# Optimization experiments

Hardware: AMD Instinct MI355X
Metric: run time of the kernel (lower is better)

## Reference

```python
import jax, jax.numpy as jnp
import numpy as np

N = 50000          # nodes (num_sensors)
E = 600000         # edges
IN_DIM = 75        # 3 * 25
DIMS = [(75, 128), (128, 128), (128, 32)]  # (in, out) per layer: in->hidden->hidden->bottleneck


def setup_inputs() -> dict:
    key = jax.random.key(0)
    ks = jax.random.split(key, 4 + 5 * len(DIMS))
    inp = {
        "x": jax.random.normal(ks[0], (N, IN_DIM), dtype=jnp.float32),
        "edge_index": jax.random.randint(ks[1], (2, E), 0, N, dtype=jnp.int64),
        "weight": jax.random.uniform(ks[2], (E,), dtype=jnp.float32),
        "sim": jax.random.normal(ks[3], (E, 2), dtype=jnp.float32),
    }
    i = 4
    for l, (cin, cout) in enumerate(DIMS):
        s = jnp.float32(1.0 / np.sqrt(cin))
        inp[f"wr{l}"] = jax.random.normal(ks[i + 0], (cin, cout), dtype=jnp.float32) * s  # real part of complex conv filter
        inp[f"wi{l}"] = jax.random.normal(ks[i + 1], (cin, cout), dtype=jnp.float32) * s  # imag part
        inp[f"cb{l}"] = jnp.zeros((cout,), dtype=jnp.float32)                              # conv bias
        inp[f"lw{l}"] = jax.random.normal(ks[i + 2], (cout, cin), dtype=jnp.float32) * s  # Linear weight (torch layout [out,in])
        inp[f"lb{l}"] = jnp.zeros((cout,), dtype=jnp.float32)                              # Linear bias
        i += 5
    return inp


def _layer(x, src, dst, cr, ci, wr, wi, cb, lw, lb):
    # ModeConvFast: gather source features, scale by complex edge coefficient
    # c = weight * (sim_r + i*sim_i), scatter-add to destination nodes,
    # project with complex filter W = wr + i*wi, keep real part, add bias.
    xs = x[src]                                   # [E, Cin] gather
    agg_r = jax.ops.segment_sum(xs * cr[:, None], dst, num_segments=N)  # [N, Cin]
    agg_i = jax.ops.segment_sum(xs * ci[:, None], dst, num_segments=N)  # [N, Cin]
    conv = agg_r @ wr - agg_i @ wi + cb           # real part of complex matmul
    return jax.nn.relu(conv + x @ lw.T + lb)      # conv(x,...) + lin(x), then relu


def reference(x, edge_index, weight, sim,
              wr0, wi0, cb0, lw0, lb0,
              wr1, wi1, cb1, lw1, lb1,
              wr2, wi2, cb2, lw2, lb2):
    src, dst = edge_index[0], edge_index[1]
    cr = weight * sim[:, 0]                       # [E] real edge coefficient
    ci = weight * sim[:, 1]                       # [E] imag edge coefficient
    layers = [
        (wr0, wi0, cb0, lw0, lb0),
        (wr1, wi1, cb1, lw1, lb1),
        (wr2, wi2, cb2, lw2, lb2),
    ]
    for p in layers:
        x = _layer(x, src, dst, cr, ci, *p)
    return x
```

## Files before the change

### kernel.cpp

```cpp
#include <hip/hip_runtime.h>

#define N_NODES 50000
#define N_EDGES 600000
#define E_PAD_MAX (N_EDGES + N_NODES * 7)

using bf16x8 = __attribute__((ext_vector_type(8))) short;
using f32x4  = __attribute__((ext_vector_type(4))) float;
typedef unsigned int uint32_tt;

__device__ __forceinline__ unsigned short f2bf(float f) {
    union { float f; unsigned int u; } v; v.f = f;
    unsigned int u = v.u;
    return (unsigned short)((u + 0x7fffu + ((u >> 16) & 1u)) >> 16);
}
__device__ __forceinline__ float bf2f(unsigned int h16) {
    union { unsigned int u; float f; } v; v.u = h16 << 16;
    return v.f;
}

__global__ void prep_kernel(
    const float* __restrict__ x0, unsigned short* __restrict__ xb,
    const float* __restrict__ wr0, const float* __restrict__ wi0,
    const float* __restrict__ lw0, unsigned short* __restrict__ BT0,
    const float* __restrict__ wr1, const float* __restrict__ wi1,
    const float* __restrict__ lw1, unsigned short* __restrict__ BT1,
    const float* __restrict__ wr2, const float* __restrict__ wi2,
    const float* __restrict__ lw2, unsigned short* __restrict__ BT2,
    int* __restrict__ cnt, uint2* __restrict__ edat, int n) {
    int tid = blockIdx.x * 256 + threadIdx.x;
    int nth = gridDim.x * 256;
    for (int i = tid; i < N_NODES; i += nth) cnt[i] = 0;
    uint2 z; z.x = 0u; z.y = 0u;
    for (int i = tid; i < E_PAD_MAX; i += nth) edat[i] = z;

    int i = tid;
    int nconv = n * 96;
    if (i < nconv) {
        int r = i / 96, c = i - r * 96;
        xb[i] = (c < 75) ? f2bf(x0[r * 75 + c]) : (unsigned short)0;
        return;
    }
    i -= nconv;
    if (i < 128 * 288) {
        int nn = i / 288, k = i - nn * 288;
        int part = k / 96, kk = k - part * 96;
        float v = 0.f;
        if (kk < 75) {
            if (part == 0)      v = wr0[kk * 128 + nn];
            else if (part == 1) v = -wi0[kk * 128 + nn];
            else                v = lw0[nn * 75 + kk];
        }
        BT0[i] = f2bf(v);
        return;
    }
    i -= 128 * 288;
    if (i < 128 * 384) {
        int nn = i / 384, k = i - nn * 384;
        int part = k >> 7, kk = k & 127;
        float v;
        if (part == 0)      v = wr1[kk * 128 + nn];
        else if (part == 1) v = -wi1[kk * 128 + nn];
        else                v = lw1[nn * 128 + kk];
        BT1[i] = f2bf(v);
        return;
    }
    i -= 128 * 384;
    if (i < 96 * 128) {
        int nn = i >> 7, k = i & 127;
        float v;
        if (nn < 32)      v = wr2[k * 32 + nn];
        else if (nn < 64) v = -wi2[k * 32 + (nn - 32)];
        else              v = lw2[(nn - 64) * 128 + k];
        BT2[i] = f2bf(v);
    }
}


__global__ void hist_kernel(const int* __restrict__ ei, int* __restrict__ cnt,
                            int* __restrict__ rank, int E) {
    int e = blockIdx.x * 256 + threadIdx.x;
    if (e < E) rank[e] = atomicAdd(&cnt[ei[E + e]], 1);
}

__global__ void scan1(const int* __restrict__ deg, int* __restrict__ out,
                      int* __restrict__ bsum, int n) {
    __shared__ int s[256];
    int t = threadIdx.x;
    int base = blockIdx.x * 1024 + t * 4;
    int v0 = (base + 0 < n) ? ((deg[base + 0] + 7) & ~7) : 0;
    int v1 = (base + 1 < n) ? ((deg[base + 1] + 7) & ~7) : 0;
    int v2 = (base + 2 < n) ? ((deg[base + 2] + 7) & ~7) : 0;
    int v3 = (base + 3 < n) ? ((deg[base + 3] + 7) & ~7) : 0;
    int tsum = v0 + v1 + v2 + v3;
    s[t] = tsum;
    __syncthreads();
    for (int off = 1; off < 256; off <<= 1) {
        int tmp = (t >= off) ? s[t - off] : 0;
        __syncthreads();
        s[t] += tmp;
        __syncthreads();
    }
    int excl = s[t] - tsum;
    if (base + 0 < n) out[base + 0] = excl;
    if (base + 1 < n) out[base + 1] = excl + v0;
    if (base + 2 < n) out[base + 2] = excl + v0 + v1;
    if (base + 3 < n) out[base + 3] = excl + v0 + v1 + v2;
    if (t == 255) bsum[blockIdx.x] = s[255];
}

__global__ void scan2(int* __restrict__ bsum, int nb) {
    if (threadIdx.x == 0 && blockIdx.x == 0) {
        int acc = 0;
        for (int i = 0; i < nb; ++i) { int v = bsum[i]; bsum[i] = acc; acc += v; }
        bsum[nb] = acc;
    }
}

__global__ void scan3(int* __restrict__ off, const int* __restrict__ bsum, int n, int nb) {
    int i = blockIdx.x * 256 + threadIdx.x;
    if (i < n) off[i] += bsum[i >> 10];
    if (i == n) off[n] = bsum[nb];
}

__global__ void scatter_kernel(const int* __restrict__ ei, const float* __restrict__ w,
                               const float* __restrict__ sim, const int* __restrict__ off,
                               const int* __restrict__ rank, uint2* __restrict__ edat,
                               int E) {
    int e = blockIdx.x * 256 + threadIdx.x;
    if (e >= E) return;
    int s = ei[e], d = ei[E + e];
    int p = off[d] + rank[e];
    float wt = w[e];
    uint2 m;
    m.x = (unsigned)s;
    m.y = (uint32_tt)f2bf(wt * sim[2 * e]) |
          ((uint32_tt)f2bf(wt * sim[2 * e + 1]) << 16);
    edat[p] = m;
}

template <int CU2>
__global__ __launch_bounds__(256) void agg_bf16(
    const uint32_tt* __restrict__ x, const int* __restrict__ off,
    const uint2* __restrict__ edat, uint32_tt* __restrict__ aggR,
    uint32_tt* __restrict__ aggI, int n) {
    int wave = threadIdx.x >> 6;
    int lane = threadIdx.x & 63;
    int node = __builtin_amdgcn_readfirstlane(blockIdx.x * 4 + wave);
    if (node >= n) return;
    int lc = (CU2 == 64) ? lane : (lane < CU2 ? lane : CU2 - 1);
    float arl = 0.f, arh = 0.f, ail = 0.f, aih = 0.f;
    int e0 = __builtin_amdgcn_readfirstlane(off[node]);
    int e1 = __builtin_amdgcn_readfirstlane(off[node + 1]);

    if (e0 < e1) {
        uint2 mn[8];
        int sc[8]; float crc[8], cic[8];
        uint32_tt wc[8];
        {
            uint2 m0[8];
#pragma unroll
            for (int j = 0; j < 8; ++j) m0[j] = edat[e0 + j];
#pragma unroll
            for (int j = 0; j < 8; ++j) {
                sc[j] = __builtin_amdgcn_readfirstlane((int)m0[j].x);
                int pk = __builtin_amdgcn_readfirstlane((int)m0[j].y);
                crc[j] = bf2f((unsigned)pk & 0xffffu);
                cic[j] = bf2f((unsigned)pk >> 16);
            }
            int nb = (e0 + 8 < e1) ? e0 + 8 : e0;
#pragma unroll
            for (int j = 0; j < 8; ++j) mn[j] = edat[nb + j];
#pragma unroll
            for (int j = 0; j < 8; ++j) wc[j] = x[(size_t)sc[j] * CU2 + lc];
        }
        for (int e = e0;; e += 8) {
            bool more = (e + 8 < e1);
            int sn[8]; float crn[8], cin_[8]; uint32_tt wn[8];
            if (more) {
#pragma unroll
                for (int j = 0; j < 8; ++j) {
                    sn[j] = __builtin_amdgcn_readfirstlane((int)mn[j].x);
                    int pk = __builtin_amdgcn_readfirstlane((int)mn[j].y);
                    crn[j] = bf2f((unsigned)pk & 0xffffu);
                    cin_[j] = bf2f((unsigned)pk >> 16);
                }
                int nb = (e + 16 < e1) ? e + 16 : e + 8;
#pragma unroll
                for (int j = 0; j < 8; ++j) mn[j] = edat[nb + j];
#pragma unroll
                for (int j = 0; j < 8; ++j) wn[j] = x[(size_t)sn[j] * CU2 + lc];
            }
#pragma unroll
            for (int j = 0; j < 8; ++j) {
                float lo = bf2f(wc[j] & 0xffffu), hi = bf2f(wc[j] >> 16);
                arl += crc[j] * lo; arh += crc[j] * hi;
                ail += cic[j] * lo; aih += cic[j] * hi;
            }
            if (!more) break;
#pragma unroll
            for (int j = 0; j < 8; ++j) {
                sc[j] = sn[j]; crc[j] = crn[j]; cic[j] = cin_[j]; wc[j] = wn[j];
            }
        }
    }
    if (lane < CU2) {
        aggR[(size_t)node * CU2 + lane] = (uint32_tt)f2bf(arl) | ((uint32_tt)f2bf(arh) << 16);
        aggI[(size_t)node * CU2 + lane] = (uint32_tt)f2bf(ail) | ((uint32_tt)f2bf(aih) << 16);
    }
}

__global__ __launch_bounds__(256) void agg_out(
    const uint32_tt* __restrict__ Y, const int* __restrict__ off,
    const uint2* __restrict__ edat, const float* __restrict__ cb,
    const float* __restrict__ lb, float* __restrict__ out, int n) {
    int wave = threadIdx.x >> 6;
    int lane = threadIdx.x & 63;
    int node = __builtin_amdgcn_readfirstlane(blockIdx.x * 4 + wave);
    if (node >= n) return;
    int lc = (lane < 32) ? lane : 31;
    int usei = (lane >> 4) & 1;
    float alo = 0.f, ahi = 0.f;
    int e0 = __builtin_amdgcn_readfirstlane(off[node]);
    int e1 = __builtin_amdgcn_readfirstlane(off[node + 1]);

    if (e0 < e1) {
        uint2 mn[8];
        int sc[8]; float crc[8], cic[8];
        uint32_tt wc[8];
        {
            uint2 m0[8];
#pragma unroll
            for (int j = 0; j < 8; ++j) m0[j] = edat[e0 + j];
#pragma unroll
            for (int j = 0; j < 8; ++j) {
                sc[j] = __builtin_amdgcn_readfirstlane((int)m0[j].x);
                int pk = __builtin_amdgcn_readfirstlane((int)m0[j].y);
                crc[j] = bf2f((unsigned)pk & 0xffffu);
                cic[j] = bf2f((unsigned)pk >> 16);
            }
            int nb = (e0 + 8 < e1) ? e0 + 8 : e0;
#pragma unroll
            for (int j = 0; j < 8; ++j) mn[j] = edat[nb + j];
#pragma unroll
            for (int j = 0; j < 8; ++j) wc[j] = Y[(size_t)sc[j] * 48 + lc];
        }
        for (int e = e0;; e += 8) {
            bool more = (e + 8 < e1);
            int sn[8]; float crn[8], cin_[8]; uint32_tt wn[8];
            if (more) {
#pragma unroll
                for (int j = 0; j < 8; ++j) {
                    sn[j] = __builtin_amdgcn_readfirstlane((int)mn[j].x);
                    int pk = __builtin_amdgcn_readfirstlane((int)mn[j].y);
                    crn[j] = bf2f((unsigned)pk & 0xffffu);
                    cin_[j] = bf2f((unsigned)pk >> 16);
                }
                int nb = (e + 16 < e1) ? e + 16 : e + 8;
#pragma unroll
                for (int j = 0; j < 8; ++j) mn[j] = edat[nb + j];
#pragma unroll
                for (int j = 0; j < 8; ++j) wn[j] = Y[(size_t)sn[j] * 48 + lc];
            }
#pragma unroll
            for (int j = 0; j < 8; ++j) {
                float c = usei ? cic[j] : crc[j];
                float lo = bf2f(wc[j] & 0xffffu), hi = bf2f(wc[j] >> 16);
                alo += c * lo; ahi += c * hi;
            }
            if (!more) break;
#pragma unroll
            for (int j = 0; j < 8; ++j) {
                sc[j] = sn[j]; crc[j] = crn[j]; cic[j] = cin_[j]; wc[j] = wn[j];
            }
        }
    }
    alo += __shfl_xor(alo, 16);
    ahi += __shfl_xor(ahi, 16);
    if (lane < 16) {
        uint32_tt lin = Y[(size_t)node * 48 + 32 + lane];
        int c0 = 2 * lane, c1 = 2 * lane + 1;
        float v0 = alo + bf2f(lin & 0xffffu) + cb[c0] + lb[c0];
        float v1 = ahi + bf2f(lin >> 16) + cb[c1] + lb[c1];
        float2 r;
        r.x = v0 > 0.f ? v0 : 0.f;
        r.y = v1 > 0.f ? v1 : 0.f;
        ((float2*)out)[(size_t)node * 16 + lane] = r;
    }
}

template <int CINP, int COUT, int BM, int WM, int WN, int MT, int NT,
          bool OUT_BF16, bool RAW, int PARTS>
__global__ __launch_bounds__(256) void gemm_mfma(
    const unsigned short* __restrict__ A0, const unsigned short* __restrict__ A1,
    const unsigned short* __restrict__ A2, const unsigned short* __restrict__ BT,
    const float* __restrict__ cb, const float* __restrict__ lb,
    void* __restrict__ outv, int n) {
    constexpr int PK = 40;
    constexpr int KTOT = PARTS * CINP;
    constexpr int NCH = KTOT / 32;
    constexpr int CPP = CINP / 32;
    __shared__ unsigned short sA[BM][PK];
    __shared__ unsigned short sB[COUT][PK];

    int t = threadIdx.x;
    int lane = t & 63, wave = t >> 6;
    int wm = wave / WN, wn = wave % WN;
    int ml = lane & 15, kh = lane >> 4;
    int node0 = blockIdx.x * BM;

    const unsigned short* Asrc[3] = {A0, A1, A2};

    f32x4 acc[MT][NT];
#pragma unroll
    for (int mt = 0; mt < MT; ++mt)
#pragma unroll
        for (int nt = 0; nt < NT; ++nt) acc[mt][nt] = (f32x4){0.f, 0.f, 0.f, 0.f};

    for (int c = 0; c < NCH; ++c) {
        int part = (PARTS == 1) ? 0 : (c / CPP);
        int kk = (c - part * CPP) * 32;
        const unsigned short* __restrict__ Ap = Asrc[part];
        __syncthreads();
#pragma unroll
        for (int i = t; i < BM * 4; i += 256) {
            int r = i >> 2, q = i & 3;
            int node = node0 + r;
            if (node >= n) node = n - 1;
            *(uint4*)&sA[r][q * 8] =
                *(const uint4*)(Ap + (size_t)node * CINP + kk + q * 8);
        }
#pragma unroll
        for (int i = t; i < COUT * 4; i += 256) {
            int r = i >> 2, q = i & 3;
            *(uint4*)&sB[r][q * 8] =
                *(const uint4*)(BT + (size_t)r * KTOT + c * 32 + q * 8);
        }
        __syncthreads();
        bf16x8 af[MT], bfr[NT];
#pragma unroll
        for (int mt = 0; mt < MT; ++mt)
            af[mt] = *(const bf16x8*)&sA[wm * (MT * 16) + mt * 16 + ml][kh * 8];
#pragma unroll
        for (int nt = 0; nt < NT; ++nt)
            bfr[nt] = *(const bf16x8*)&sB[wn * (NT * 16) + nt * 16 + ml][kh * 8];
#pragma unroll
        for (int mt = 0; mt < MT; ++mt)
#pragma unroll
            for (int nt = 0; nt < NT; ++nt)
                acc[mt][nt] = __builtin_amdgcn_mfma_f32_16x16x32_bf16(
                    af[mt], bfr[nt], acc[mt][nt], 0, 0, 0);
    }

    int row0 = kh * 4;
#pragma unroll
    for (int nt = 0; nt < NT; ++nt) {
        int col = wn * (NT * 16) + nt * 16 + ml;
        float bias = RAW ? 0.f : (cb[col] + lb[col]);
#pragma unroll
        for (int mt = 0; mt < MT; ++mt) {
#pragma unroll
            for (int r = 0; r < 4; ++r) {
                int node = node0 + wm * (MT * 16) + mt * 16 + row0 + r;
                if (node < n) {
                    float v = acc[mt][nt][r] + bias;
                    if (!RAW) v = v > 0.f ? v : 0.f;
                    if (OUT_BF16)
                        ((unsigned short*)outv)[(size_t)node * COUT + col] = f2bf(v);
                    else
                        ((float*)outv)[(size_t)node * COUT + col] = v;
                }
            }
        }
    }
}


extern "C" void kernel_launch(void* const* d_in, const int* in_sizes, int n_in,
                              void* d_out, int out_size, void* d_ws, size_t ws_size,
                              hipStream_t stream) {
    const float* x0  = (const float*)d_in[0];
    const int*   ei  = (const int*)d_in[1];
    const float* wgt = (const float*)d_in[2];
    const float* sim = (const float*)d_in[3];
    const float *wr[3], *wi[3], *cb[3], *lw[3], *lb[3];
    for (int l = 0; l < 3; ++l) {
        wr[l] = (const float*)d_in[4 + 5 * l];
        wi[l] = (const float*)d_in[5 + 5 * l];
        cb[l] = (const float*)d_in[6 + 5 * l];
        lw[l] = (const float*)d_in[7 + 5 * l];
        lb[l] = (const float*)d_in[8 + 5 * l];
    }

    char* p = (char*)d_ws;
    auto alloc = [&](size_t bytes) -> void* {
        void* r = p;
        p += (bytes + 255) & ~(size_t)255;
        return r;
    };
    int*   off  = (int*)alloc((N_NODES + 1) * 4);
    int*   cnt  = (int*)alloc(N_NODES * 4);
    int*   bsum = (int*)alloc(256);
    int*   rank = (int*)alloc((size_t)N_EDGES * 4);
    uint2* edat = (uint2*)alloc((size_t)E_PAD_MAX * 8);
    unsigned short* xb    = (unsigned short*)alloc((size_t)N_NODES * 96 * 2);
    unsigned short* aggRb = (unsigned short*)alloc((size_t)N_NODES * 128 * 2);
    unsigned short* aggIb = (unsigned short*)alloc((size_t)N_NODES * 128 * 2);
    unsigned short* h1b   = (unsigned short*)alloc((size_t)N_NODES * 128 * 2);
    unsigned short* h2b   = (unsigned short*)alloc((size_t)N_NODES * 128 * 2);
    unsigned short* Yb    = (unsigned short*)alloc((size_t)N_NODES * 96 * 2);
    unsigned short* BT0   = (unsigned short*)alloc((size_t)128 * 288 * 2);
    unsigned short* BT1   = (unsigned short*)alloc((size_t)128 * 384 * 2);
    unsigned short* BT2   = (unsigned short*)alloc((size_t)96 * 128 * 2);
    float* outp = (float*)d_out;

    {
        int total = N_NODES * 96 + 128 * 288 + 128 * 384 + 96 * 128;
        prep_kernel<<<(total + 255) / 256, 256, 0, stream>>>(
            x0, xb, wr[0], wi[0], lw[0], BT0, wr[1], wi[1], lw[1], BT1,
            wr[2], wi[2], lw[2], BT2, cnt, edat, N_NODES);
    }
    hist_kernel<<<(N_EDGES + 255) / 256, 256, 0, stream>>>(ei, cnt, rank, N_EDGES);
    int nb = (N_NODES + 1023) / 1024;
    scan1<<<nb, 256, 0, stream>>>(cnt, off, bsum, N_NODES);
    scan2<<<1, 64, 0, stream>>>(bsum, nb);
    scan3<<<(N_NODES + 1 + 255) / 256, 256, 0, stream>>>(off, bsum, N_NODES, nb);
    scatter_kernel<<<(N_EDGES + 255) / 256, 256, 0, stream>>>(ei, wgt, sim, off, rank,
                                                              edat, N_EDGES);

    int agrid = (N_NODES + 3) / 4;

    agg_bf16<48><<<agrid, 256, 0, stream>>>((const uint32_tt*)xb, off, edat,
                                            (uint32_tt*)aggRb, (uint32_tt*)aggIb, N_NODES);
    gemm_mfma<96, 128, 128, 2, 2, 4, 4, true, false, 3>
        <<<(N_NODES + 127) / 128, 256, 0, stream>>>(aggRb, aggIb, xb, BT0, cb[0], lb[0],
                                                    h1b, N_NODES);
    agg_bf16<64><<<agrid, 256, 0, stream>>>((const uint32_tt*)h1b, off, edat,
                                            (uint32_tt*)aggRb, (uint32_tt*)aggIb, N_NODES);
    gemm_mfma<128, 128, 128, 2, 2, 4, 4, true, false, 3>
        <<<(N_NODES + 127) / 128, 256, 0, stream>>>(aggRb, aggIb, h1b, BT1, cb[1], lb[1],
                                                    h2b, N_NODES);
    gemm_mfma<128, 96, 128, 2, 2, 4, 3, true, true, 1>
        <<<(N_NODES + 127) / 128, 256, 0, stream>>>(h2b, h2b, h2b, BT2, cb[2], lb[2],
                                                    Yb, N_NODES);
    agg_out<<<agrid, 256, 0, stream>>>((const uint32_tt*)Yb, off, edat, cb[2], lb[2],
                                       outp, N_NODES);
}
```

Measured before the change: 269.9 us.

## Fuse layer-2 GEMM with Y projection, merge scan passes, split agg_out lanes

Adds a gemm_l1y kernel that computes the layer-1 hidden tile into shared memory and immediately multiplies it by the layer-2 projection weights. This removes the h2 round trip through global memory and one kernel launch. The single-thread scan2 is folded into scan3: each block now sums the preceding block totals itself, which repeats a little work per block but drops a serial launch. agg_out now uses both 32-lane halves of the wave for alternating edges, so all 64 lanes do useful loads, at the cost of one extra cross-half shuffle reduction.

```diff
diff --git a/kernel.cpp b/kernel.cpp
--- a/kernel.cpp
+++ b/kernel.cpp
@@ -108,18 +108,24 @@
     if (t == 255) bsum[blockIdx.x] = s[255];
 }
 
-__global__ void scan2(int* __restrict__ bsum, int nb) {
-    if (threadIdx.x == 0 && blockIdx.x == 0) {
+__global__ void scan3(int* __restrict__ off, const int* __restrict__ bsum,
+                      int n, int nb) {
+    __shared__ int sp;
+    int b = blockIdx.x, t = threadIdx.x;
+    int seg = b >> 2;
+    if (t == 0) {
         int acc = 0;
-        for (int i = 0; i < nb; ++i) { int v = bsum[i]; bsum[i] = acc; acc += v; }
-        bsum[nb] = acc;
-    }
-}
-
-__global__ void scan3(int* __restrict__ off, const int* __restrict__ bsum, int n, int nb) {
-    int i = blockIdx.x * 256 + threadIdx.x;
-    if (i < n) off[i] += bsum[i >> 10];
-    if (i == n) off[n] = bsum[nb];
+        for (int k = 0; k < seg; ++k) acc += bsum[k];
+        sp = acc;
+    }
+    __syncthreads();
+    int i = b * 256 + t;
+    if (i < n) off[i] += sp;
+    if (i == n) {
+        int tot = sp;
+        for (int k = seg; k < nb; ++k) tot += bsum[k];
+        off[n] = tot;
+    }
 }
 
 __global__ void scatter_kernel(const int* __restrict__ ei, const float* __restrict__ w,
@@ -217,8 +223,7 @@
     int lane = threadIdx.x & 63;
     int node = __builtin_amdgcn_readfirstlane(blockIdx.x * 4 + wave);
     if (node >= n) return;
-    int lc = (lane < 32) ? lane : 31;
-    int usei = (lane >> 4) & 1;
+    int half = lane >> 5, sl = lane & 31;
     float alo = 0.f, ahi = 0.f;
     int e0 = __builtin_amdgcn_readfirstlane(off[node]);
     int e1 = __builtin_amdgcn_readfirstlane(off[node + 1]);
@@ -226,7 +231,7 @@
     if (e0 < e1) {
         uint2 mn[8];
         int sc[8]; float crc[8], cic[8];
-        uint32_tt wc[8];
+        uint32_tt wc[4];
         {
             uint2 m0[8];
 #pragma unroll
@@ -242,11 +247,14 @@
 #pragma unroll
             for (int j = 0; j < 8; ++j) mn[j] = edat[nb + j];
 #pragma unroll
-            for (int j = 0; j < 8; ++j) wc[j] = Y[(size_t)sc[j] * 48 + lc];
+            for (int k = 0; k < 4; ++k) {
+                int sp = half ? sc[2 * k + 1] : sc[2 * k];
+                wc[k] = Y[(size_t)sp * 48 + sl];
+            }
         }
         for (int e = e0;; e += 8) {
             bool more = (e + 8 < e1);
-            int sn[8]; float crn[8], cin_[8]; uint32_tt wn[8];
+            int sn[8]; float crn[8], cin_[8]; uint32_tt wn4[4];
             if (more) {
 #pragma unroll
                 for (int j = 0; j < 8; ++j) {
@@ -259,23 +267,30 @@
 #pragma unroll
                 for (int j = 0; j < 8; ++j) mn[j] = edat[nb + j];
 #pragma unroll
-                for (int j = 0; j < 8; ++j) wn[j] = Y[(size_t)sn[j] * 48 + lc];
-            }
+                for (int k = 0; k < 4; ++k) {
+                    int sp = half ? sn[2 * k + 1] : sn[2 * k];
+                    wn4[k] = Y[(size_t)sp * 48 + sl];
+                }
+            }
+#pragma unroll
+            for (int k = 0; k < 4; ++k) {
+                float crp = half ? crc[2 * k + 1] : crc[2 * k];
+                float cip = half ? cic[2 * k + 1] : cic[2 * k];
+                float c = (sl < 16) ? crp : cip;
+                float lo = bf2f(wc[k] & 0xffffu), hi = bf2f(wc[k] >> 16);
+                alo += c * lo; ahi += c * hi;
+            }
+            if (!more) break;
 #pragma unroll
             for (int j = 0; j < 8; ++j) {
-                float c = usei ? cic[j] : crc[j];
-                float lo = bf2f(wc[j] & 0xffffu), hi = bf2f(wc[j] >> 16);
-                alo += c * lo; ahi += c * hi;
-            }
-            if (!more) break;
-#pragma unroll
-            for (int j = 0; j < 8; ++j) {
-                sc[j] = sn[j]; crc[j] = crn[j]; cic[j] = cin_[j]; wc[j] = wn[j];
-            }
-        }
-    }
-    alo += __shfl_xor(alo, 16);
-    ahi += __shfl_xor(ahi, 16);
+                sc[j] = sn[j]; crc[j] = crn[j]; cic[j] = cin_[j];
+            }
+#pragma unroll
+            for (int k = 0; k < 4; ++k) wc[k] = wn4[k];
+        }
+    }
+    alo += __shfl_xor(alo, 32); ahi += __shfl_xor(ahi, 32);
+    alo += __shfl_xor(alo, 16); ahi += __shfl_xor(ahi, 16);
     if (lane < 16) {
         uint32_tt lin = Y[(size_t)node * 48 + 32 + lane];
         int c0 = 2 * lane, c1 = 2 * lane + 1;
@@ -369,6 +384,119 @@
                     else
                         ((float*)outv)[(size_t)node * COUT + col] = v;
                 }
+            }
+        }
+    }
+}
+
+__global__ __launch_bounds__(256) void gemm_l1y(
+    const unsigned short* __restrict__ A0, const unsigned short* __restrict__ A1,
+    const unsigned short* __restrict__ A2, const unsigned short* __restrict__ BT,
+    const unsigned short* __restrict__ BT2, const float* __restrict__ cb,
+    const float* __restrict__ lb, unsigned short* __restrict__ Yout, int n) {
+    constexpr int PK = 40;
+    constexpr int PH = 136;
+    __shared__ unsigned short sA[128][PK];
+    __shared__ unsigned short sB[128][PK];
+    __shared__ unsigned short sH[128][PH];
+
+    int t = threadIdx.x;
+    int lane = t & 63, wave = t >> 6;
+    int wm = wave >> 1, wn = wave & 1;
+    int ml = lane & 15, kh = lane >> 4;
+    int node0 = blockIdx.x * 128;
+    const unsigned short* Asrc[3] = {A0, A1, A2};
+
+    f32x4 acc[4][4];
+#pragma unroll
+    for (int mt = 0; mt < 4; ++mt)
+#pragma unroll
+        for (int nt = 0; nt < 4; ++nt) acc[mt][nt] = (f32x4){0.f, 0.f, 0.f, 0.f};
+
+    for (int c = 0; c < 12; ++c) {
+        int part = c >> 2;
+        int kk = (c & 3) * 32;
+        const unsigned short* __restrict__ Ap = Asrc[part];
+        __syncthreads();
+#pragma unroll
+        for (int i = t; i < 512; i += 256) {
+            int r = i >> 2, q = i & 3;
+            int node = node0 + r;
+            if (node >= n) node = n - 1;
+            *(uint4*)&sA[r][q * 8] =
+                *(const uint4*)(Ap + (size_t)node * 128 + kk + q * 8);
+        }
+#pragma unroll
+        for (int i = t; i < 512; i += 256) {
+            int r = i >> 2, q = i & 3;
+            *(uint4*)&sB[r][q * 8] =
+                *(const uint4*)(BT + (size_t)r * 384 + c * 32 + q * 8);
+        }
+        __syncthreads();
+        bf16x8 af[4], bfr[4];
+#pragma unroll
+        for (int mt = 0; mt < 4; ++mt)
+            af[mt] = *(const bf16x8*)&sA[wm * 64 + mt * 16 + ml][kh * 8];
+#pragma unroll
+        for (int nt = 0; nt < 4; ++nt)
+            bfr[nt] = *(const bf16x8*)&sB[wn * 64 + nt * 16 + ml][kh * 8];
+#pragma unroll
+        for (int mt = 0; mt < 4; ++mt)
+#pragma unroll
+            for (int nt = 0; nt < 4; ++nt)
+                acc[mt][nt] = __builtin_amdgcn_mfma_f32_16x16x32_bf16(
+                    af[mt], bfr[nt], acc[mt][nt], 0, 0, 0);
+    }
+
+    int row0 = kh * 4;
+#pragma unroll
+    for (int nt = 0; nt < 4; ++nt) {
+        int col = wn * 64 + nt * 16 + ml;
+        float bias = cb[col] + lb[col];
+#pragma unroll
+        for (int mt = 0; mt < 4; ++mt) {
+#pragma unroll
+            for (int r = 0; r < 4; ++r) {
+                int nl = wm * 64 + mt * 16 + row0 + r;
+                float v = acc[mt][nt][r] + bias;
+                sH[nl][col] = f2bf(v > 0.f ? v : 0.f);
+            }
+        }
+    }
+    __syncthreads();
+
+    f32x4 acc2[4][3];
+#pragma unroll
+    for (int mt = 0; mt < 4; ++mt)
+#pragma unroll
+        for (int nt = 0; nt < 3; ++nt) acc2[mt][nt] = (f32x4){0.f, 0.f, 0.f, 0.f};
+    for (int c2 = 0; c2 < 4; ++c2) {
+        bf16x8 af[4], bfr[3];
+#pragma unroll
+        for (int mt = 0; mt < 4; ++mt)
+            af[mt] = *(const bf16x8*)&sH[wm * 64 + mt * 16 + ml][c2 * 32 + kh * 8];
+#pragma unroll
+        for (int nt = 0; nt < 3; ++nt) {
+            int ycol = wn * 48 + nt * 16 + ml;
+            bfr[nt] = *(const bf16x8*)(BT2 + (size_t)ycol * 128 + c2 * 32 + kh * 8);
+        }
+#pragma unroll
+        for (int mt = 0; mt < 4; ++mt)
+#pragma unroll
+            for (int nt = 0; nt < 3; ++nt)
+                acc2[mt][nt] = __builtin_amdgcn_mfma_f32_16x16x32_bf16(
+                    af[mt], bfr[nt], acc2[mt][nt], 0, 0, 0);
+    }
+#pragma unroll
+    for (int nt = 0; nt < 3; ++nt) {
+        int ycol = wn * 48 + nt * 16 + ml;
+#pragma unroll
+        for (int mt = 0; mt < 4; ++mt) {
+#pragma unroll
+            for (int r = 0; r < 4; ++r) {
+                int node = node0 + wm * 64 + mt * 16 + row0 + r;
+                if (node < n)
+                    Yout[(size_t)node * 96 + ycol] = f2bf(acc2[mt][nt][r]);
             }
         }
     }
@@ -406,7 +534,6 @@
     unsigned short* aggRb = (unsigned short*)alloc((size_t)N_NODES * 128 * 2);
     unsigned short* aggIb = (unsigned short*)alloc((size_t)N_NODES * 128 * 2);
     unsigned short* h1b   = (unsigned short*)alloc((size_t)N_NODES * 128 * 2);
-    unsigned short* h2b   = (unsigned short*)alloc((size_t)N_NODES * 128 * 2);
     unsigned short* Yb    = (unsigned short*)alloc((size_t)N_NODES * 96 * 2);
     unsigned short* BT0   = (unsigned short*)alloc((size_t)128 * 288 * 2);
     unsigned short* BT1   = (unsigned short*)alloc((size_t)128 * 384 * 2);
@@ -422,7 +549,6 @@
     hist_kernel<<<(N_EDGES + 255) / 256, 256, 0, stream>>>(ei, cnt, rank, N_EDGES);
     int nb = (N_NODES + 1023) / 1024;
     scan1<<<nb, 256, 0, stream>>>(cnt, off, bsum, N_NODES);
-    scan2<<<1, 64, 0, stream>>>(bsum, nb);
     scan3<<<(N_NODES + 1 + 255) / 256, 256, 0, stream>>>(off, bsum, N_NODES, nb);
     scatter_kernel<<<(N_EDGES + 255) / 256, 256, 0, stream>>>(ei, wgt, sim, off, rank,
                                                               edat, N_EDGES);
@@ -436,12 +562,8 @@
                                                     h1b, N_NODES);
     agg_bf16<64><<<agrid, 256, 0, stream>>>((const uint32_tt*)h1b, off, edat,
                                             (uint32_tt*)aggRb, (uint32_tt*)aggIb, N_NODES);
-    gemm_mfma<128, 128, 128, 2, 2, 4, 4, true, false, 3>
-        <<<(N_NODES + 127) / 128, 256, 0, stream>>>(aggRb, aggIb, h1b, BT1, cb[1], lb[1],
-                                                    h2b, N_NODES);
-    gemm_mfma<128, 96, 128, 2, 2, 4, 3, true, true, 1>
-        <<<(N_NODES + 127) / 128, 256, 0, stream>>>(h2b, h2b, h2b, BT2, cb[2], lb[2],
-                                                    Yb, N_NODES);
+    gemm_l1y<<<(N_NODES + 127) / 128, 256, 0, stream>>>(aggRb, aggIb, h1b, BT1, BT2,
+                                                        cb[1], lb[1], Yb, N_NODES);
     agg_out<<<agrid, 256, 0, stream>>>((const uint32_tt*)Yb, off, edat, cb[2], lb[2],
                                        outp, N_NODES);
 }
```

Measured after the change: 287.3 us. 1.06x slower.
